# Optimization experiments

Hardware: AMD Instinct MI355X
Metric: run time of the kernel (lower is better)

## Reference

```python
import jax, jax.numpy as jnp
import numpy as np

B, D, T, R = 64, 256, 24, 17  # batch, nef, max words, region grid
GAMMA1, GAMMA2, GAMMA3 = 4.0, 5.0, 10.0
EPS = 1e-8
NEG = -1e30  # stand-in for -inf (safe for softmax + grads)


def setup_inputs() -> dict:
    key = jax.random.key(0)
    k1, k2, k3, k4 = jax.random.split(key, 4)
    img_features = jax.random.normal(k1, (B, D, R, R), dtype=jnp.float32)
    words_emb = jax.random.normal(k2, (B, D, T), dtype=jnp.float32)
    cap_lens = jax.random.randint(k3, (B,), 4, T + 1)  # lengths in [4, T]
    class_ids = jax.random.randint(k4, (B,), 0, 20)
    labels = jnp.arange(B, dtype=jnp.int32)
    return {"img_features": img_features, "words_emb": words_emb,
            "labels": labels, "cap_lens": cap_lens, "class_ids": class_ids}


def reference(img_features, words_emb, labels, cap_lens, class_ids):
    S = R * R
    ctx = img_features.reshape(B, D, S)                    # [b,d,s]
    tmask = jnp.arange(T)[None, :] < cap_lens[:, None]     # [i,t] valid words

    # func_attention, vectorized over query sample i and context image b
    attn = jnp.einsum('bds,idt->ibst', ctx, words_emb)     # [i,b,s,t]
    attn = jnp.where(tmask[:, None, None, :], attn, NEG)
    attn = jax.nn.softmax(attn, axis=3)                    # softmax over words
    attn = attn.transpose(0, 1, 3, 2) * GAMMA1             # [i,b,t,s]
    attn = jax.nn.softmax(attn, axis=3)                    # softmax over regions
    wei = jnp.einsum('bds,ibts->ibdt', ctx, attn)          # weighted context [i,b,d,t]

    # cosine similarity word vs weighted context, per word position
    w = words_emb[:, None, :, :]                           # [i,1,d,t]
    num = jnp.sum(w * wei, axis=2)                         # [i,b,t]
    den = (jnp.linalg.norm(w, axis=2) * jnp.linalg.norm(wei, axis=2)).clip(EPS)
    row_sim = num / den                                    # [i,b,t]

    # masked exp-sum-log over valid words
    e = jnp.where(tmask[:, None, :], jnp.exp(GAMMA2 * row_sim), 0.0)
    sims = jnp.log(jnp.sum(e, axis=2))                     # [i,b]
    similarities = sims.T * GAMMA3                         # [b,i] (torch cats per-i columns)

    # mask same-class pairs (excluding diagonal)
    cmask = (class_ids[None, :] == class_ids[:, None]) & ~jnp.eye(B, dtype=bool)
    similarities = jnp.where(cmask, NEG, similarities)

    idx = jnp.arange(B)
    loss0 = -jnp.mean(jax.nn.log_softmax(similarities, axis=1)[idx, labels])
    loss1 = -jnp.mean(jax.nn.log_softmax(similarities.T, axis=1)[idx, labels])

    att_maps = attn[idx, idx].reshape(B, T, R, R)          # padded attention maps
    return loss0, loss1, att_maps
```

## Files before the change

### kernel.cpp

```cpp
#include <hip/hip_runtime.h>
#include <math.h>

namespace {
constexpr int Bn = 64;
constexpr int Dn = 256;
constexpr int Tn = 24;
constexpr int Rn = 17;
constexpr int Sn = Rn * Rn;
constexpr float G1 = 4.0f, G2 = 5.0f, G3 = 10.0f;
constexpr float EPSF = 1e-8f;
constexpr float NEGF = -1e30f;
constexpr int MT_A = 19;
constexpr int KK_A = 8;
constexpr int DT_B = 16;
constexpr int KK_B = 10;
constexpr int ESTR = 344;
constexpr int PSTR = 305;
constexpr int TSTR = 293;
constexpr int WSTR = 24;
constexpr int ASTR = 24;
constexpr int NT = 320;
}

typedef __attribute__((ext_vector_type(8))) short bf16x8;
typedef __attribute__((ext_vector_type(4))) float f32x4;

#define MFMA_BF16 __builtin_amdgcn_mfma_f32_16x16x32_bf16

__device__ __forceinline__ short f2bf(float x) {
  unsigned u = __float_as_uint(x);
  return (short)((u + 0x7FFFu + ((u >> 16) & 1u)) >> 16);
}
__device__ __forceinline__ float bf2f(short h) {
  return __uint_as_float(((unsigned)(unsigned short)h) << 16);
}

__global__ __launch_bounds__(256) void kprep_ctx(const float* __restrict__ ctx,
                                                 short* __restrict__ Ahf,
                                                 short* __restrict__ Alf,
                                                 short* __restrict__ Chf,
                                                 short* __restrict__ Clf) {
  __shared__ float tile[32][TSTR];
  const int b = blockIdx.x >> 3;
  const int d0b = blockIdx.x & 7;
  const int d0 = d0b * 32;
  const int tid = threadIdx.x;
  const int tx = tid & 31, ty = tid >> 5;

  for (int r = ty; r < 32; r += 8) {
    const float* src = ctx + ((size_t)b * Dn + d0 + r) * Sn;
    for (int s = tx; s < Sn; s += 32) tile[r][s] = src[s];
  }
  __syncthreads();

  for (int slot = tid; slot < MT_A * 64; slot += 256) {
    const int mt = slot >> 6;
    const int lane = slot & 63;
    const int s = mt * 16 + (lane & 15);
    const int dl = (lane >> 4) * 8;
    bf16x8 hi, lo;
#pragma unroll
    for (int e = 0; e < 8; ++e) {
      float v = (s < Sn) ? tile[dl + e][s] : 0.f;
      short h = f2bf(v);
      hi[e] = h;
      lo[e] = f2bf(v - bf2f(h));
    }
    const size_t gid = ((size_t)(b * MT_A + mt) * KK_A + d0b) * 64 + lane;
    *(bf16x8*)&Ahf[gid * 8] = hi;
    *(bf16x8*)&Alf[gid * 8] = lo;
  }

  for (int slot = tid; slot < 2 * KK_B * 64; slot += 256) {
    const int lane = slot & 63;
    const int f = slot >> 6;
    const int kk = f % KK_B;
    const int dtl = f / KK_B;
    const int dloc = dtl * 16 + (lane & 15);
    const int s0 = kk * 32 + (lane >> 4) * 8;
    bf16x8 hi, lo;
#pragma unroll
    for (int e = 0; e < 8; ++e) {
      const int s = s0 + e;
      float v = (s < Sn) ? tile[dloc][s] : 0.f;
      short h = f2bf(v);
      hi[e] = h;
      lo[e] = f2bf(v - bf2f(h));
    }
    const size_t gid = ((size_t)(b * DT_B + (d0b * 2 + dtl)) * KK_B + kk) * 64 + lane;
    *(bf16x8*)&Chf[gid * 8] = hi;
    *(bf16x8*)&Clf[gid * 8] = lo;
  }
}

__global__ __launch_bounds__(256) void kprep_Wf(const float* __restrict__ words,
                                                short* __restrict__ Whf,
                                                short* __restrict__ Wlf) {
  const int total = Bn * KK_A * 2 * 64;
  for (int gid = blockIdx.x * 256 + threadIdx.x; gid < total; gid += gridDim.x * 256) {
    const int lane = gid & 63;
    int f = gid >> 6;
    const int n = f & 1; f >>= 1;
    const int kk = f & 7;
    const int i = f >> 3;
    const int t = n * 16 + (lane & 15);
    const int d0 = kk * 32 + (lane >> 4) * 8;
    bf16x8 hi, lo;
#pragma unroll
    for (int e = 0; e < 8; ++e) {
      float v = (t < Tn) ? words[((size_t)i * Dn + d0 + e) * Tn + t] : 0.f;
      short h = f2bf(v);
      hi[e] = h;
      lo[e] = f2bf(v - bf2f(h));
    }
    *(bf16x8*)&Whf[(size_t)gid * 8] = hi;
    *(bf16x8*)&Wlf[(size_t)gid * 8] = lo;
  }
}

__global__ __launch_bounds__(512, 6) void k_main8(
    const short* __restrict__ Ahf, const short* __restrict__ Alf,
    const short* __restrict__ Chf, const short* __restrict__ Clf,
    const short* __restrict__ Whf, const short* __restrict__ Wlf,
    const float* __restrict__ words, const int* __restrict__ cap_lens,
    float* __restrict__ sims, float* __restrict__ att_out)
{
  __shared__ __align__(16) short U[2][32][ESTR];
  __shared__ float inv2s[32];
  __shared__ float redN[Tn], redV[Tn], redW[Tn], redE[Tn];
  float (*P)[PSTR] = (float (*)[PSTR]) & U[0][0][0];

  const int bid = blockIdx.x;
  const int i = bid & 63, b = bid >> 6;
  const int tid = threadIdx.x;
  const int lane = tid & 63;
  const int wv = tid >> 6;
  const int l15 = lane & 15, lg = lane >> 4;
  const int len = cap_lens[i];

  if (tid < Tn) { redN[tid] = 0.f; redV[tid] = 0.f; redW[tid] = 0.f; }

  f32x4 acc[3][2];
#pragma unroll
  for (int j = 0; j < 3; ++j) {
    acc[j][0] = f32x4{0.f, 0.f, 0.f, 0.f};
    acc[j][1] = f32x4{0.f, 0.f, 0.f, 0.f};
  }
#pragma unroll 2
  for (int kk = 0; kk < KK_A; ++kk) {
    const size_t Wb = ((size_t)(i * KK_A + kk) * 2) * 512 + (size_t)lane * 8;
    bf16x8 bh0 = *(const bf16x8*)&Whf[Wb];
    bf16x8 bl0 = *(const bf16x8*)&Wlf[Wb];
    bf16x8 bh1 = *(const bf16x8*)&Whf[Wb + 512];
    bf16x8 bl1 = *(const bf16x8*)&Wlf[Wb + 512];
#pragma unroll
    for (int j = 0; j < 3; ++j) {
      const int mt = wv + j * 8;
      if (mt < MT_A) {
        const size_t Ab = ((size_t)(b * MT_A + mt) * KK_A + kk) * 512 + (size_t)lane * 8;
        bf16x8 ah = *(const bf16x8*)&Ahf[Ab];
        bf16x8 al = *(const bf16x8*)&Alf[Ab];
        __builtin_amdgcn_s_setprio(1);
        acc[j][0] = MFMA_BF16(ah, bh0, acc[j][0], 0, 0, 0);
        acc[j][0] = MFMA_BF16(ah, bl0, acc[j][0], 0, 0, 0);
        acc[j][0] = MFMA_BF16(al, bh0, acc[j][0], 0, 0, 0);
        acc[j][1] = MFMA_BF16(ah, bh1, acc[j][1], 0, 0, 0);
        acc[j][1] = MFMA_BF16(ah, bl1, acc[j][1], 0, 0, 0);
        acc[j][1] = MFMA_BF16(al, bh1, acc[j][1], 0, 0, 0);
        __builtin_amdgcn_s_setprio(0);
      }
    }
  }

  const int t0 = l15, t1 = 16 + l15;
#pragma unroll
  for (int j = 0; j < 3; ++j) {
    const int mt = wv + j * 8;
    if (mt >= MT_A) continue;
    float mx[4], e0[4], e1[4], sum[4];
#pragma unroll
    for (int q = 0; q < 4; ++q) {
      float a = (t0 < len) ? acc[j][0][q] : NEGF;
      float c = (t1 < len) ? acc[j][1][q] : NEGF;
      mx[q] = fmaxf(a, c);
    }
#pragma unroll
    for (int q = 0; q < 4; ++q) {
      mx[q] = fmaxf(mx[q], __shfl_xor(mx[q], 1));
      mx[q] = fmaxf(mx[q], __shfl_xor(mx[q], 2));
      mx[q] = fmaxf(mx[q], __shfl_xor(mx[q], 4));
      mx[q] = fmaxf(mx[q], __shfl_xor(mx[q], 8));
    }
#pragma unroll
    for (int q = 0; q < 4; ++q) {
      e0[q] = (t0 < len) ? __expf(acc[j][0][q] - mx[q]) : 0.f;
      e1[q] = (t1 < len) ? __expf(acc[j][1][q] - mx[q]) : 0.f;
      sum[q] = e0[q] + e1[q];
    }
#pragma unroll
    for (int q = 0; q < 4; ++q) {
      sum[q] += __shfl_xor(sum[q], 1);
      sum[q] += __shfl_xor(sum[q], 2);
      sum[q] += __shfl_xor(sum[q], 4);
      sum[q] += __shfl_xor(sum[q], 8);
    }
#pragma unroll
    for (int q = 0; q < 4; ++q) {
      const int s = mt * 16 + lg * 4 + q;
      const float inv = 1.f / sum[q];
      if (s < Sn) {
        P[t0][s] = e0[q] * inv;
        if (l15 < 8) P[t1][s] = e1[q] * inv;
      }
    }
  }
  __syncthreads();

  const int t2 = tid >> 4;
  const int g2i = tid & 15;
  float ev[19];
  float sinv = 0.f;
  if (t2 < Tn) {
    float mx = NEGF;
#pragma unroll
    for (int k = 0; k < 19; ++k) {
      const int s = g2i + 16 * k;
      ev[k] = (s < Sn) ? P[t2][s] : NEGF;
      mx = fmaxf(mx, ev[k]);
    }
    mx = fmaxf(mx, __shfl_xor(mx, 1));
    mx = fmaxf(mx, __shfl_xor(mx, 2));
    mx = fmaxf(mx, __shfl_xor(mx, 4));
    mx = fmaxf(mx, __shfl_xor(mx, 8));
    mx *= G1;
    float sum = 0.f;
#pragma unroll
    for (int k = 0; k < 19; ++k) {
      const int s = g2i + 16 * k;
      float e = (s < Sn) ? __expf(G1 * ev[k] - mx) : 0.f;
      ev[k] = e;
      sum += e;
    }
    sum += __shfl_xor(sum, 1);
    sum += __shfl_xor(sum, 2);
    sum += __shfl_xor(sum, 4);
    sum += __shfl_xor(sum, 8);
    sinv = 1.f / sum;
    if (g2i == 0) inv2s[t2] = sinv;
  }
  __syncthreads();

  if (t2 < Tn) {
#pragma unroll
    for (int k = 0; k < 19; ++k) {
      const int s = g2i + 16 * k;
      if (s < Sn) {
        float e = ev[k];
        short h = f2bf(e);
        U[0][t2][s] = h;
        U[1][t2][s] = f2bf(e - bf2f(h));
      }
    }
    if (i == b) {
      float* ao = att_out + ((size_t)i * Tn + t2) * Sn;
#pragma unroll
      for (int k = 0; k < 19; ++k) {
        const int s = g2i + 16 * k;
        if (s < Sn) ao[s] = ev[k] * sinv;
      }
    }
  }
  for (int idx = tid; idx < 24 * 31; idx += 512) {
    const int r = idx / 31, c = 289 + idx % 31;
    U[0][r][c] = 0; U[1][r][c] = 0;
  }
  for (int idx = tid; idx < 8 * ESTR; idx += 512) {
    const int r = 24 + idx / ESTR, c = idx % ESTR;
    U[0][r][c] = 0; U[1][r][c] = 0;
  }
  __syncthreads();

  f32x4 acc2[2][2];
#pragma unroll
  for (int j = 0; j < 2; ++j) {
    acc2[j][0] = f32x4{0.f, 0.f, 0.f, 0.f};
    acc2[j][1] = f32x4{0.f, 0.f, 0.f, 0.f};
  }
#pragma unroll 2
  for (int kk = 0; kk < KK_B; ++kk) {
    const int k0 = kk * 32 + lg * 8;
    bf16x8 bh0 = *(const bf16x8*)&U[0][l15][k0];
    bf16x8 bl0 = *(const bf16x8*)&U[1][l15][k0];
    bf16x8 bh1 = *(const bf16x8*)&U[0][16 + l15][k0];
    bf16x8 bl1 = *(const bf16x8*)&U[1][16 + l15][k0];
#pragma unroll
    for (int j = 0; j < 2; ++j) {
      const int dt = wv + j * 8;
      const size_t Cb = ((size_t)(b * DT_B + dt) * KK_B + kk) * 512 + (size_t)lane * 8;
      bf16x8 ah = *(const bf16x8*)&Chf[Cb];
      bf16x8 al = *(const bf16x8*)&Clf[Cb];
      __builtin_amdgcn_s_setprio(1);
      acc2[j][0] = MFMA_BF16(ah, bh0, acc2[j][0], 0, 0, 0);
      acc2[j][0] = MFMA_BF16(ah, bl0, acc2[j][0], 0, 0, 0);
      acc2[j][0] = MFMA_BF16(al, bh0, acc2[j][0], 0, 0, 0);
      acc2[j][1] = MFMA_BF16(ah, bh1, acc2[j][1], 0, 0, 0);
      acc2[j][1] = MFMA_BF16(ah, bl1, acc2[j][1], 0, 0, 0);
      acc2[j][1] = MFMA_BF16(al, bh1, acc2[j][1], 0, 0, 0);
      __builtin_amdgcn_s_setprio(0);
    }
  }

  float pn[2] = {0.f, 0.f}, pv[2] = {0.f, 0.f}, pw[2] = {0.f, 0.f};
#pragma unroll
  for (int nt = 0; nt < 2; ++nt) {
    const int t = nt * 16 + l15;
    const bool tv = (t < Tn);
    const float iv = tv ? inv2s[t] : 0.f;
#pragma unroll
    for (int j = 0; j < 2; ++j) {
#pragma unroll
      for (int q = 0; q < 4; ++q) {
        const int d = (wv + j * 8) * 16 + lg * 4 + q;
        const float wei = acc2[j][nt][q] * iv;
        const float wvv = tv ? words[((size_t)i * Dn + d) * Tn + t] : 0.f;
        pn[nt] = fmaf(wvv, wei, pn[nt]);
        pv[nt] = fmaf(wei, wei, pv[nt]);
        pw[nt] = fmaf(wvv, wvv, pw[nt]);
      }
    }
  }
#pragma unroll
  for (int nt = 0; nt < 2; ++nt) {
    pn[nt] += __shfl_xor(pn[nt], 16); pn[nt] += __shfl_xor(pn[nt], 32);
    pv[nt] += __shfl_xor(pv[nt], 16); pv[nt] += __shfl_xor(pv[nt], 32);
    pw[nt] += __shfl_xor(pw[nt], 16); pw[nt] += __shfl_xor(pw[nt], 32);
  }
  if (lg == 0) {
#pragma unroll
    for (int nt = 0; nt < 2; ++nt) {
      const int t = nt * 16 + l15;
      if (t < Tn) {
        atomicAdd(&redN[t], pn[nt]);
        atomicAdd(&redV[t], pv[nt]);
        atomicAdd(&redW[t], pw[nt]);
      }
    }
  }
  __syncthreads();
  if (tid < Tn) {
    const float den = fmaxf(sqrtf(redW[tid]) * sqrtf(redV[tid]), EPSF);
    const float rs = redN[tid] / den;
    redE[tid] = (tid < len) ? __expf(G2 * rs) : 0.f;
  }
  __syncthreads();
  if (tid == 0) {
    float ssum = 0.f;
#pragma unroll
    for (int t = 0; t < Tn; ++t) ssum += redE[t];
    sims[i * Bn + b] = logf(ssum);
  }
}

__device__ __forceinline__ void fma24(float v, const float* __restrict__ row,
                                      float* __restrict__ acc) {
#pragma unroll
  for (int t = 0; t < Tn; ++t) acc[t] = fmaf(v, row[t], acc[t]);
}

__global__ __launch_bounds__(256) void k_transpose(const float* __restrict__ ctx,
                                                   float* __restrict__ ctxT) {
  __shared__ float tile[32][33];
  const int b = blockIdx.z;
  const int x0 = blockIdx.x * 32;
  const int y0 = blockIdx.y * 32;
  const int tx = threadIdx.x, ty = threadIdx.y;
  const float* src = ctx + (size_t)b * Dn * Sn;
  float* dst = ctxT + (size_t)b * Sn * Dn;
#pragma unroll
  for (int k = 0; k < 4; ++k) {
    int y = y0 + ty + k * 8, x = x0 + tx;
    if (x < Sn) tile[ty + k * 8][tx] = src[(size_t)y * Sn + x];
  }
  __syncthreads();
#pragma unroll
  for (int k = 0; k < 4; ++k) {
    int x = x0 + ty + k * 8, y = y0 + tx;
    if (x < Sn) dst[(size_t)x * Dn + y] = tile[tx][ty + k * 8];
  }
}

__global__ __launch_bounds__(NT) void k_main_valu(
    const float* __restrict__ ctx, const float* __restrict__ words,
    const float* __restrict__ g2, int tstr, int sstr,
    const int* __restrict__ cap_lens,
    float* __restrict__ sims, float* __restrict__ att_out)
{
  __shared__ __align__(16) float Wl[Dn * WSTR];
  __shared__ __align__(16) float AT[Sn * ASTR];
  __shared__ float inv2[Tn];
  __shared__ float red[Tn];

  const int bid = blockIdx.x;
  const int i = bid & 63, b = bid >> 6;
  const int tid = threadIdx.x;
  const int len = cap_lens[i];

  {
    const float4* wsrc = (const float4*)(words + (size_t)i * Dn * Tn);
    float4* wdst = (float4*)Wl;
    for (int k = tid; k < Dn * Tn / 4; k += NT) wdst[k] = wsrc[k];
  }
  __syncthreads();

  if (tid < Sn) {
    float acc[Tn];
#pragma unroll
    for (int t = 0; t < Tn; ++t) acc[t] = 0.f;
    const float* cb = ctx + (size_t)b * Dn * Sn + tid;
    float v0 = cb[0], v1 = cb[Sn];
    int d = 0;
    for (; d < Dn - 2; d += 2) {
      float n0 = cb[(size_t)(d + 2) * Sn];
      float n1 = cb[(size_t)(d + 3) * Sn];
      fma24(v0, &Wl[d * WSTR], acc);
      fma24(v1, &Wl[(d + 1) * WSTR], acc);
      v0 = n0; v1 = n1;
    }
    fma24(v0, &Wl[d * WSTR], acc);
    fma24(v1, &Wl[(d + 1) * WSTR], acc);
    float m = NEGF;
#pragma unroll
    for (int t = 0; t < Tn; ++t)
      if (t < len) m = fmaxf(m, acc[t]);
    float sum = 0.f;
#pragma unroll
    for (int t = 0; t < Tn; ++t) {
      float e = (t < len) ? __expf(acc[t] - m) : 0.f;
      acc[t] = e; sum += e;
    }
    const float inv = 1.f / sum;
#pragma unroll
    for (int t = 0; t < Tn; ++t) AT[tid * ASTR + t] = acc[t] * inv;
  }
  __syncthreads();

  if (tid < Tn * 8) {
    const int t = tid >> 3, g = tid & 7;
    float m = NEGF;
    for (int ss = g; ss < Sn; ss += 8) m = fmaxf(m, AT[ss * ASTR + t]);
    m = fmaxf(m, __shfl_xor(m, 1));
    m = fmaxf(m, __shfl_xor(m, 2));
    m = fmaxf(m, __shfl_xor(m, 4));
    m *= G1;
    float sum = 0.f;
    for (int ss = g; ss < Sn; ss += 8) {
      float e = __expf(G1 * AT[ss * ASTR + t] - m);
      AT[ss * ASTR + t] = e;
      sum += e;
    }
    sum += __shfl_xor(sum, 1);
    sum += __shfl_xor(sum, 2);
    sum += __shfl_xor(sum, 4);
    if (g == 0) inv2[t] = 1.f / sum;
  }
  __syncthreads();

  float acc2[Tn];
  if (tid < Dn) {
#pragma unroll
    for (int t = 0; t < Tn; ++t) acc2[t] = 0.f;
    const float* src = g2 + (size_t)b * Dn * Sn + (size_t)tid * tstr;
    const size_t s1 = sstr, s2 = 2 * (size_t)sstr, s3 = 3 * (size_t)sstr,
                 s4 = 4 * (size_t)sstr;
    float p0 = src[0], p1 = src[s1], p2 = src[s2], p3 = src[s3];
    const float* nsrc = src + s4;
    int ss = 0;
    for (; ss < 284; ss += 4) {
      float n0 = nsrc[0], n1 = nsrc[s1], n2 = nsrc[s2], n3 = nsrc[s3];
      fma24(p0, &AT[ss * ASTR], acc2);
      fma24(p1, &AT[(ss + 1) * ASTR], acc2);
      fma24(p2, &AT[(ss + 2) * ASTR], acc2);
      fma24(p3, &AT[(ss + 3) * ASTR], acc2);
      p0 = n0; p1 = n1; p2 = n2; p3 = n3;
      nsrc += s4;
    }
    fma24(p0, &AT[284 * ASTR], acc2);
    fma24(p1, &AT[285 * ASTR], acc2);
    fma24(p2, &AT[286 * ASTR], acc2);
    fma24(p3, &AT[287 * ASTR], acc2);
    {
      float v = src[(size_t)288 * sstr];
      fma24(v, &AT[288 * ASTR], acc2);
    }
#pragma unroll
    for (int t = 0; t < Tn; ++t) acc2[t] *= inv2[t];
  }

  if (i == b) {
#pragma unroll 1
    for (int t = 0; t < Tn; ++t) {
      const float iv = inv2[t];
      for (int ss = tid; ss < Sn; ss += NT)
        att_out[(size_t)i * Tn * Sn + (size_t)t * Sn + ss] = AT[ss * ASTR + t] * iv;
    }
  }
  __syncthreads();

  if (tid < Dn) {
#pragma unroll
    for (int t = 0; t < Tn; ++t) AT[tid * ASTR + t] = acc2[t];
  }
  __syncthreads();

  if (tid < Tn * 8) {
    const int t = tid >> 3, g = tid & 7;
    float num = 0.f, wn = 0.f, vn = 0.f;
    for (int dd = g; dd < Dn; dd += 8) {
      float wvv = Wl[dd * WSTR + t];
      float uv = AT[dd * ASTR + t];
      num = fmaf(wvv, uv, num);
      wn = fmaf(wvv, wvv, wn);
      vn = fmaf(uv, uv, vn);
    }
    num += __shfl_xor(num, 1); num += __shfl_xor(num, 2); num += __shfl_xor(num, 4);
    wn  += __shfl_xor(wn, 1);  wn  += __shfl_xor(wn, 2);  wn  += __shfl_xor(wn, 4);
    vn  += __shfl_xor(vn, 1);  vn  += __shfl_xor(vn, 2);  vn  += __shfl_xor(vn, 4);
    if (g == 0) {
      float den = fmaxf(sqrtf(wn) * sqrtf(vn), EPSF);
      float rs = num / den;
      red[t] = (t < len) ? __expf(G2 * rs) : 0.f;
    }
  }
  __syncthreads();

  if (tid == 0) {
    float ssum = 0.f;
#pragma unroll
    for (int t = 0; t < Tn; ++t) ssum += red[t];
    sims[i * Bn + b] = logf(ssum);
  }
}

__global__ __launch_bounds__(64) void k_loss(const float* __restrict__ sims,
                                             const int* __restrict__ labels,
                                             const int* __restrict__ class_ids,
                                             float* __restrict__ out) {
  const int r = threadIdx.x;
  const int cr = class_ids[r];
  const int lab = labels[r];

  float m0 = NEGF;
  for (int c = 0; c < Bn; ++c) {
    float v = sims[c * Bn + r] * G3;
    if (class_ids[c] == cr && c != r) v = NEGF;
    m0 = fmaxf(m0, v);
  }
  float se0 = 0.f, tgt0 = 0.f;
  for (int c = 0; c < Bn; ++c) {
    float v = sims[c * Bn + r] * G3;
    if (class_ids[c] == cr && c != r) v = NEGF;
    se0 += __expf(v - m0);
    if (c == lab) tgt0 = v;
  }
  float val0 = tgt0 - (m0 + logf(se0));

  float m1 = NEGF;
  for (int c = 0; c < Bn; ++c) {
    float v = sims[r * Bn + c] * G3;
    if (class_ids[c] == cr && c != r) v = NEGF;
    m1 = fmaxf(m1, v);
  }
  float se1 = 0.f, tgt1 = 0.f;
  for (int c = 0; c < Bn; ++c) {
    float v = sims[r * Bn + c] * G3;
    if (class_ids[c] == cr && c != r) v = NEGF;
    se1 += __expf(v - m1);
    if (c == lab) tgt1 = v;
  }
  float val1 = tgt1 - (m1 + logf(se1));

  for (int off = 1; off < 64; off <<= 1) {
    val0 += __shfl_xor(val0, off);
    val1 += __shfl_xor(val1, off);
  }
  if (r == 0) {
    out[0] = -val0 / (float)Bn;
    out[1] = -val1 / (float)Bn;
  }
}

extern "C" void kernel_launch(void* const* d_in, const int* in_sizes, int n_in,
                              void* d_out, int out_size, void* d_ws, size_t ws_size,
                              hipStream_t stream) {
  const float* img      = (const float*)d_in[0];
  const float* words    = (const float*)d_in[1];
  const int*   labels   = (const int*)d_in[2];
  const int*   cap_lens = (const int*)d_in[3];
  const int*   class_ids= (const int*)d_in[4];
  float* out = (float*)d_out;

  float* sims = (float*)d_ws;
  size_t off = (size_t)Bn * Bn * sizeof(float);
  const size_t AhB = (size_t)Bn * MT_A * KK_A * 512 * 2;
  const size_t ChB = (size_t)Bn * DT_B * KK_B * 512 * 2;
  const size_t WhB = (size_t)Bn * KK_A * 2 * 512 * 2;
  short* Ahf = (short*)((char*)d_ws + off); off += AhB;
  short* Alf = (short*)((char*)d_ws + off); off += AhB;
  short* Chf = (short*)((char*)d_ws + off); off += ChB;
  short* Clf = (short*)((char*)d_ws + off); off += ChB;
  short* Whf = (short*)((char*)d_ws + off); off += WhB;
  short* Wlf = (short*)((char*)d_ws + off); off += WhB;

  if (ws_size >= off) {
    kprep_ctx<<<Bn * 8, 256, 0, stream>>>(img, Ahf, Alf, Chf, Clf);
    kprep_Wf<<<(Bn * KK_A * 2 * 64 + 255) / 256, 256, 0, stream>>>(words, Whf, Wlf);
    k_main8<<<Bn * Bn, 512, 0, stream>>>(Ahf, Alf, Chf, Clf, Whf, Wlf,
                                         words, cap_lens, sims, out + 2);
  } else {
    const size_t simsB = (size_t)Bn * Bn * sizeof(float);
    const size_t ctxTB = (size_t)Bn * Sn * Dn * sizeof(float);
    float* ctxT = (float*)((char*)d_ws + simsB);
    const bool useT = ws_size >= simsB + ctxTB;
    const float* g2 = img;
    int tstr = Sn, sstr = 1;
    if (useT) {
      dim3 tb(32, 8);
      dim3 tg((Sn + 31) / 32, Dn / 32, Bn);
      k_transpose<<<tg, tb, 0, stream>>>(img, ctxT);
      g2 = ctxT; tstr = 1; sstr = Dn;
    }
    k_main_valu<<<Bn * Bn, NT, 0, stream>>>(img, words, g2, tstr, sstr,
                                            cap_lens, sims, out + 2);
  }

  k_loss<<<1, 64, 0, stream>>>(sims, labels, class_ids, out);
}
```

Measured before the change: 268.2 us.

## Merge word prep into ctx prep and fuse loss via last-block counter

Folds the word-embedding bf16 split kernel into the context prep kernel as extra blocks, and computes the final contrastive loss inside the main kernel using an atomic completion counter so the last block finishes the reduction. Together these remove two kernel launches from the fast path. The main MFMA loops are also fully unrolled. This adds a threadfence and atomic per block, serial loss work on one block at the tail, and possibly higher register pressure from the unrolling.

```diff
diff --git a/kernel.cpp b/kernel.cpp
--- a/kernel.cpp
+++ b/kernel.cpp
@@ -36,15 +36,46 @@
 }
 
 __global__ __launch_bounds__(256) void kprep_ctx(const float* __restrict__ ctx,
+                                                 const float* __restrict__ words,
                                                  short* __restrict__ Ahf,
                                                  short* __restrict__ Alf,
                                                  short* __restrict__ Chf,
-                                                 short* __restrict__ Clf) {
+                                                 short* __restrict__ Clf,
+                                                 short* __restrict__ Whf,
+                                                 short* __restrict__ Wlf,
+                                                 unsigned* __restrict__ cnt) {
   __shared__ float tile[32][TSTR];
+  const int tid = threadIdx.x;
+  if (blockIdx.x == 0 && tid == 0) *cnt = 0u;
+
+  if (blockIdx.x >= Bn * 8) {
+    const int wb = blockIdx.x - Bn * 8;
+    const int total = Bn * KK_A * 2 * 64;
+    for (int gid = wb * 256 + tid; gid < total; gid += 8 * 256) {
+      const int lane = gid & 63;
+      int f = gid >> 6;
+      const int n = f & 1; f >>= 1;
+      const int kk = f & 7;
+      const int i = f >> 3;
+      const int t = n * 16 + (lane & 15);
+      const int d0 = kk * 32 + (lane >> 4) * 8;
+      bf16x8 hi, lo;
+#pragma unroll
+      for (int e = 0; e < 8; ++e) {
+        float v = (t < Tn) ? words[((size_t)i * Dn + d0 + e) * Tn + t] : 0.f;
+        short h = f2bf(v);
+        hi[e] = h;
+        lo[e] = f2bf(v - bf2f(h));
+      }
+      *(bf16x8*)&Whf[(size_t)gid * 8] = hi;
+      *(bf16x8*)&Wlf[(size_t)gid * 8] = lo;
+    }
+    return;
+  }
+
   const int b = blockIdx.x >> 3;
   const int d0b = blockIdx.x & 7;
   const int d0 = d0b * 32;
-  const int tid = threadIdx.x;
   const int tx = tid & 31, ty = tid >> 5;
 
   for (int r = ty; r < 32; r += 8) {
@@ -93,41 +124,19 @@
   }
 }
 
-__global__ __launch_bounds__(256) void kprep_Wf(const float* __restrict__ words,
-                                                short* __restrict__ Whf,
-                                                short* __restrict__ Wlf) {
-  const int total = Bn * KK_A * 2 * 64;
-  for (int gid = blockIdx.x * 256 + threadIdx.x; gid < total; gid += gridDim.x * 256) {
-    const int lane = gid & 63;
-    int f = gid >> 6;
-    const int n = f & 1; f >>= 1;
-    const int kk = f & 7;
-    const int i = f >> 3;
-    const int t = n * 16 + (lane & 15);
-    const int d0 = kk * 32 + (lane >> 4) * 8;
-    bf16x8 hi, lo;
-#pragma unroll
-    for (int e = 0; e < 8; ++e) {
-      float v = (t < Tn) ? words[((size_t)i * Dn + d0 + e) * Tn + t] : 0.f;
-      short h = f2bf(v);
-      hi[e] = h;
-      lo[e] = f2bf(v - bf2f(h));
-    }
-    *(bf16x8*)&Whf[(size_t)gid * 8] = hi;
-    *(bf16x8*)&Wlf[(size_t)gid * 8] = lo;
-  }
-}
-
 __global__ __launch_bounds__(512, 6) void k_main8(
     const short* __restrict__ Ahf, const short* __restrict__ Alf,
     const short* __restrict__ Chf, const short* __restrict__ Clf,
     const short* __restrict__ Whf, const short* __restrict__ Wlf,
     const float* __restrict__ words, const int* __restrict__ cap_lens,
-    float* __restrict__ sims, float* __restrict__ att_out)
+    const int* __restrict__ labels, const int* __restrict__ class_ids,
+    unsigned* __restrict__ cnt,
+    float* __restrict__ sims, float* __restrict__ out, float* __restrict__ att_out)
 {
   __shared__ __align__(16) short U[2][32][ESTR];
   __shared__ float inv2s[32];
   __shared__ float redN[Tn], redV[Tn], redW[Tn], redE[Tn];
+  __shared__ unsigned lastflag;
   float (*P)[PSTR] = (float (*)[PSTR]) & U[0][0][0];
 
   const int bid = blockIdx.x;
@@ -146,7 +155,7 @@
     acc[j][0] = f32x4{0.f, 0.f, 0.f, 0.f};
     acc[j][1] = f32x4{0.f, 0.f, 0.f, 0.f};
   }
-#pragma unroll 2
+#pragma unroll
   for (int kk = 0; kk < KK_A; ++kk) {
     const size_t Wb = ((size_t)(i * KK_A + kk) * 2) * 512 + (size_t)lane * 8;
     bf16x8 bh0 = *(const bf16x8*)&Whf[Wb];
@@ -286,7 +295,7 @@
     acc2[j][0] = f32x4{0.f, 0.f, 0.f, 0.f};
     acc2[j][1] = f32x4{0.f, 0.f, 0.f, 0.f};
   }
-#pragma unroll 2
+#pragma unroll
   for (int kk = 0; kk < KK_B; ++kk) {
     const int k0 = kk * 32 + lg * 8;
     bf16x8 bh0 = *(const bf16x8*)&U[0][l15][k0];
@@ -358,6 +367,59 @@
 #pragma unroll
     for (int t = 0; t < Tn; ++t) ssum += redE[t];
     sims[i * Bn + b] = logf(ssum);
+  }
+  __syncthreads();
+
+  if (tid == 0) {
+    __threadfence();
+    unsigned old = atomicAdd(cnt, 1u);
+    lastflag = (old == (unsigned)(Bn * Bn - 1)) ? 1u : 0u;
+  }
+  __syncthreads();
+  if (lastflag && tid < 64) {
+    __threadfence();
+    const int r = tid;
+    const int cr = class_ids[r];
+    const int lab = labels[r];
+
+    float m0 = NEGF;
+    for (int c = 0; c < Bn; ++c) {
+      float v = sims[c * Bn + r] * G3;
+      if (class_ids[c] == cr && c != r) v = NEGF;
+      m0 = fmaxf(m0, v);
+    }
+    float se0 = 0.f, tgt0 = 0.f;
+    for (int c = 0; c < Bn; ++c) {
+      float v = sims[c * Bn + r] * G3;
+      if (class_ids[c] == cr && c != r) v = NEGF;
+      se0 += __expf(v - m0);
+      if (c == lab) tgt0 = v;
+    }
+    float val0 = tgt0 - (m0 + logf(se0));
+
+    float m1 = NEGF;
+    for (int c = 0; c < Bn; ++c) {
+      float v = sims[r * Bn + c] * G3;
+      if (class_ids[c] == cr && c != r) v = NEGF;
+      m1 = fmaxf(m1, v);
+    }
+    float se1 = 0.f, tgt1 = 0.f;
+    for (int c = 0; c < Bn; ++c) {
+      float v = sims[r * Bn + c] * G3;
+      if (class_ids[c] == cr && c != r) v = NEGF;
+      se1 += __expf(v - m1);
+      if (c == lab) tgt1 = v;
+    }
+    float val1 = tgt1 - (m1 + logf(se1));
+
+    for (int off = 1; off < 64; off <<= 1) {
+      val0 += __shfl_xor(val0, off);
+      val1 += __shfl_xor(val1, off);
+    }
+    if (r == 0) {
+      out[0] = -val0 / (float)Bn;
+      out[1] = -val1 / (float)Bn;
+    }
   }
 }
 
@@ -610,12 +672,14 @@
   short* Clf = (short*)((char*)d_ws + off); off += ChB;
   short* Whf = (short*)((char*)d_ws + off); off += WhB;
   short* Wlf = (short*)((char*)d_ws + off); off += WhB;
+  unsigned* cnt = (unsigned*)((char*)d_ws + off); off += 256;
 
   if (ws_size >= off) {
-    kprep_ctx<<<Bn * 8, 256, 0, stream>>>(img, Ahf, Alf, Chf, Clf);
-    kprep_Wf<<<(Bn * KK_A * 2 * 64 + 255) / 256, 256, 0, stream>>>(words, Whf, Wlf);
+    kprep_ctx<<<Bn * 8 + 8, 256, 0, stream>>>(img, words, Ahf, Alf, Chf, Clf,
+                                              Whf, Wlf, cnt);
     k_main8<<<Bn * Bn, 512, 0, stream>>>(Ahf, Alf, Chf, Clf, Whf, Wlf,
-                                         words, cap_lens, sims, out + 2);
+                                         words, cap_lens, labels, class_ids,
+                                         cnt, sims, out, out + 2);
   } else {
     const size_t simsB = (size_t)Bn * Bn * sizeof(float);
     const size_t ctxTB = (size_t)Bn * Sn * Dn * sizeof(float);
@@ -631,7 +695,6 @@
     }
     k_main_valu<<<Bn * Bn, NT, 0, stream>>>(img, words, g2, tstr, sstr,
                                             cap_lens, sims, out + 2);
-  }
-
-  k_loss<<<1, 64, 0, stream>>>(sims, labels, class_ids, out);
-}
+    k_loss<<<1, 64, 0, stream>>>(sims, labels, class_ids, out);
+  }
+}
```

After: 402.7 us. +50.2%, slower.
